# Performance work log

Hardware: AMD Instinct MI355X
Metric: run time of the kernel (lower is better)

## Reference

```python
import jax, jax.numpy as jnp
import numpy as np

T, B = 64, 256
VOCAB, D, H = 32000, 512, 1024


def setup_inputs() -> dict:
    key = jax.random.key(0)
    k1, k2, k3, k4 = jax.random.split(key, 4)
    x = jax.random.randint(k1, (T, B), 0, VOCAB)  # token 0 = padding
    embed = jax.random.normal(k2, (VOCAB, D), dtype=jnp.float32)
    w_i = jax.random.normal(k3, (D, 3 * H), dtype=jnp.float32) / np.sqrt(D)
    w_h = jax.random.normal(k4, (H, 3 * H), dtype=jnp.float32) / np.sqrt(H)
    b = jnp.zeros((3 * H,), dtype=jnp.float32)
    return {"x": x, "embed": embed, "w_i": w_i, "w_h": w_h, "b": b}


def reference(x, embed, w_i, w_h, b):
    # Embed and mask out padding token 0.  words: [T, B, D]
    words = embed[x] * (x > 0).astype(embed.dtype)[..., None]
    h_dim = w_h.shape[0]
    w_h_zr, w_h_a = w_h[:, : 2 * h_dim], w_h[:, 2 * h_dim :]
    b_zr, b_a = b[: 2 * h_dim], b[2 * h_dim :]

    def step(h, w_t):
        gx = w_t @ w_i  # [B, 3H]
        zr_x, a_x = gx[..., : 2 * h_dim], gx[..., 2 * h_dim :]
        zr = jax.nn.sigmoid(zr_x + h @ w_h_zr + b_zr)
        z, r = zr[..., :h_dim], zr[..., h_dim:]
        a = jnp.tanh(a_x + (r * h) @ w_h_a + b_a)
        h_new = (1.0 - z) * h + z * a
        return h_new, h_new

    h0 = jnp.zeros((x.shape[1], h_dim), dtype=embed.dtype)
    _, seq = jax.lax.scan(step, h0, words)  # seq: [T, B, H]
    return seq.sum(0)  # compress == 'sum' -> [B, H]
```

## Files before the change

### kernel.cpp

```cpp
#include <hip/hip_runtime.h>
#include <hip/hip_bf16.h>
#include <stdint.h>


#define TT 64
#define BB 256
#define DD 512
#define HH 1024
#define N3H 3072

using frag  = __attribute__((ext_vector_type(8))) short;
using f32x4 = __attribute__((ext_vector_type(4))) float;

__device__ __forceinline__ uint16_t f2b(float f) {
    uint32_t u = __builtin_bit_cast(uint32_t, f);
    uint32_t r = u + 0x7FFFu + ((u >> 16) & 1u);
    return (uint16_t)(r >> 16);
}
__device__ __forceinline__ float b2f(uint16_t b) {
    uint32_t u = ((uint32_t)b) << 16;
    return __builtin_bit_cast(float, u);
}

__device__ __forceinline__ void load8_l3(const uint16_t* p, frag* f) {
    asm volatile(
        "global_load_dwordx4 %0, %8, off sc0 sc1\n\t"
        "global_load_dwordx4 %1, %8, off offset:64 sc0 sc1\n\t"
        "global_load_dwordx4 %2, %8, off offset:128 sc0 sc1\n\t"
        "global_load_dwordx4 %3, %8, off offset:192 sc0 sc1\n\t"
        "global_load_dwordx4 %4, %8, off offset:256 sc0 sc1\n\t"
        "global_load_dwordx4 %5, %8, off offset:320 sc0 sc1\n\t"
        "global_load_dwordx4 %6, %8, off offset:384 sc0 sc1\n\t"
        "global_load_dwordx4 %7, %8, off offset:448 sc0 sc1\n\t"
        "s_waitcnt vmcnt(0)"
        : "=&v"(f[0]), "=&v"(f[1]), "=&v"(f[2]), "=&v"(f[3]),
          "=&v"(f[4]), "=&v"(f[5]), "=&v"(f[6]), "=&v"(f[7])
        : "v"(p)
        : "memory");
}


__global__ __launch_bounds__(256) void k_gather(const int* __restrict__ x,
                                                const float* __restrict__ embed,
                                                uint16_t* __restrict__ words) {
    int tid = blockIdx.x * 256 + threadIdx.x;
    int row = tid >> 6;
    int c8  = (tid & 63) << 3;
    int tok = x[row];
    float s = (tok > 0) ? 1.f : 0.f;
    const float4* src = (const float4*)(embed + (int64_t)tok * DD + c8);
    float4 v0 = src[0], v1 = src[1];
    float vals[8] = {v0.x, v0.y, v0.z, v0.w, v1.x, v1.y, v1.z, v1.w};
    union { uint16_t u[8]; uint4 q; } pk;
#pragma unroll
    for (int i = 0; i < 8; ++i) pk.u[i] = f2b(vals[i] * s);
    *(uint4*)(words + ((int64_t)row << 9) + c8) = pk.q;
}

__global__ void k_transpose(const float* __restrict__ src, uint16_t* __restrict__ dst,
                            int K, int N) {
    __shared__ float tile[32][33];
    int n0 = blockIdx.x * 32, k0 = blockIdx.y * 32;
    int tx = threadIdx.x, ty = threadIdx.y;
#pragma unroll
    for (int i = 0; i < 32; i += 8)
        tile[ty + i][tx] = src[(int64_t)(k0 + ty + i) * N + n0 + tx];
    __syncthreads();
#pragma unroll
    for (int i = 0; i < 32; i += 8)
        dst[(int64_t)(n0 + ty + i) * K + k0 + tx] = f2b(tile[tx][ty + i]);
}

__global__ void k_zero(uint4* p, int n16) {
    int i = blockIdx.x * blockDim.x + threadIdx.x;
    if (i < n16) p[i] = uint4{0u, 0u, 0u, 0u};
}


__global__ __launch_bounds__(256) void k_gemm_gx(const uint16_t* __restrict__ A,
                                                 const uint16_t* __restrict__ BT,
                                                 const float* __restrict__ bias,
                                                 uint16_t* __restrict__ C) {
    __shared__ uint16_t As[128][72];
    __shared__ uint16_t Bs[128][72];
    int m0 = blockIdx.y * 128;
    int n0 = blockIdx.x * 128;
    int t = threadIdx.x;
    int wave = t >> 6, lane = t & 63, quad = lane >> 4, l16 = lane & 15;
    int wm = (wave & 1) * 64, wn = (wave >> 1) * 64;
    f32x4 acc[4][4] = {};

    int sr = t >> 1;
    int sc = (t & 1) * 32;

    for (int k0 = 0; k0 < DD; k0 += 64) {
        const uint4* ga = (const uint4*)(A + (int64_t)(m0 + sr) * DD + k0 + sc);
        uint4 a0 = ga[0], a1 = ga[1], a2 = ga[2], a3 = ga[3];
        const uint4* gb = (const uint4*)(BT + (int64_t)(n0 + sr) * DD + k0 + sc);
        uint4 b0 = gb[0], b1 = gb[1], b2 = gb[2], b3 = gb[3];
        __syncthreads();
        *(uint4*)&As[sr][sc]      = a0;
        *(uint4*)&As[sr][sc + 8]  = a1;
        *(uint4*)&As[sr][sc + 16] = a2;
        *(uint4*)&As[sr][sc + 24] = a3;
        *(uint4*)&Bs[sr][sc]      = b0;
        *(uint4*)&Bs[sr][sc + 8]  = b1;
        *(uint4*)&Bs[sr][sc + 16] = b2;
        *(uint4*)&Bs[sr][sc + 24] = b3;
        __syncthreads();
#pragma unroll
        for (int kk = 0; kk < 64; kk += 32) {
            frag af[4], bf[4];
#pragma unroll
            for (int mi = 0; mi < 4; ++mi)
                af[mi] = *(const frag*)&As[wm + mi * 16 + l16][kk + quad * 8];
#pragma unroll
            for (int ni = 0; ni < 4; ++ni)
                bf[ni] = *(const frag*)&Bs[wn + ni * 16 + l16][kk + quad * 8];
#pragma unroll
            for (int mi = 0; mi < 4; ++mi)
#pragma unroll
                for (int ni = 0; ni < 4; ++ni)
                    acc[mi][ni] = __builtin_amdgcn_mfma_f32_16x16x32_bf16(
                        af[mi], bf[ni], acc[mi][ni], 0, 0, 0);
        }
    }
#pragma unroll
    for (int ni = 0; ni < 4; ++ni) {
        int col = n0 + wn + ni * 16 + l16;
        float bv = bias[col];
#pragma unroll
        for (int mi = 0; mi < 4; ++mi)
#pragma unroll
            for (int r = 0; r < 4; ++r) {
                int row = m0 + wm + mi * 16 + quad * 4 + r;
                C[(int64_t)row * N3H + col] = f2b(acc[mi][ni][r] + bv);
            }
    }
}


__global__ __launch_bounds__(256, 1) void k_recur(const uint16_t* __restrict__ gx,
                                                  const uint16_t* __restrict__ wht,
                                                  uint16_t* __restrict__ hbuf,
                                                  uint16_t* __restrict__ rhbuf,
                                                  unsigned int* __restrict__ bar,
                                                  float* __restrict__ out) {
    extern __shared__ uint16_t Wh[];
    const int LDW = HH + 8;
    int mg = blockIdx.x;
    int jb = blockIdx.y;
    int j0 = jb * 16;
    int m0 = mg * 64;
    int t = threadIdx.x, wave = t >> 6, lane = t & 63, quad = lane >> 4, l16 = lane & 15;

    for (int c = t; c < 48 * 128; c += 256) {
        int row = c >> 7;
        int off = (c & 127) << 3;
        int s = row >> 4, i = row & 15;
        *(uint4*)(Wh + row * LDW + off) =
            *(const uint4*)(wht + (int64_t)(s * HH + j0 + i) * HH + off);
    }
    __syncthreads();

    float hp[4]   = {0.f, 0.f, 0.f, 0.f};
    float zg[4];
    float osum[4] = {0.f, 0.f, 0.f, 0.f};
    int brow = m0 + wave * 16 + quad * 4;
    int jcol = j0 + l16;
    const int jc4 = j0 + (l16 & ~3);
    unsigned int* flags = bar + mg * 1024;
    unsigned int phase = 0;

    const uint16_t* harow  = hbuf  + (int64_t)(m0 + wave * 16 + l16) * HH + quad * 8;
    const uint16_t* rharow = rhbuf + (int64_t)(m0 + wave * 16 + l16) * HH + quad * 8;

    auto bar_arrive = [&]() {
        __syncthreads();
        if (t == 0)
            (void)__hip_atomic_fetch_add(&flags[jb * 16], 1u, __ATOMIC_RELAXED,
                                         __HIP_MEMORY_SCOPE_AGENT);
    };
    auto bar_wait = [&](unsigned int ph) {
        if (wave == 0) {
            long guard = 0;
            for (;;) {
                unsigned int v = __hip_atomic_load(&flags[lane * 16], __ATOMIC_RELAXED,
                                                   __HIP_MEMORY_SCOPE_AGENT);
                if (__all((int)(v >= ph))) break;
                __builtin_amdgcn_s_sleep(1);
                if (++guard > (1L << 13)) break;
            }
        }
        __syncthreads();
    };

    auto store4 = [&](uint16_t* base, int r, uint32_t mine) {
        uint32_t p2 = mine | (((uint32_t)__shfl_xor((int)mine, 1)) << 16);
        uint32_t hi = (uint32_t)__shfl_xor((int)p2, 2);
        if ((l16 & 3) == 0) {
            uint64_t p4 = (uint64_t)p2 | ((uint64_t)hi << 32);
            uint64_t* dst = (uint64_t*)base + (int64_t)(brow + r) * (HH / 4) + (jc4 >> 2);
            (void)__hip_atomic_exchange(dst, p4, __ATOMIC_RELAXED, __HIP_MEMORY_SCOPE_AGENT);
        }
    };

    for (int step = 0; step < TT; ++step) {
        if (step > 0) bar_arrive();

        uint16_t gzv[4], grv[4], gav[4];
        {
            const uint16_t* gxrow = gx + (int64_t)step * BB * N3H;
#pragma unroll
            for (int r = 0; r < 4; ++r) {
                const uint16_t* g = gxrow + (int64_t)(brow + r) * N3H + jcol;
                gzv[r] = g[0]; grv[r] = g[HH]; gav[r] = g[2 * HH];
            }
        }

        if (step > 0) bar_wait(++phase);

        {
            f32x4 acc0 = {}, acc1 = {};
            frag af[8];
#pragma unroll
            for (int kb = 0; kb < 4; ++kb) {
                load8_l3(harow + kb * 256, af);
#pragma unroll
                for (int j = 0; j < 8; ++j) {
                    int kk = kb * 8 + j;
                    frag b0 = *(const frag*)(Wh + (l16)      * LDW + kk * 32 + quad * 8);
                    frag b1 = *(const frag*)(Wh + (16 + l16) * LDW + kk * 32 + quad * 8);
                    acc0 = __builtin_amdgcn_mfma_f32_16x16x32_bf16(af[j], b0, acc0, 0, 0, 0);
                    acc1 = __builtin_amdgcn_mfma_f32_16x16x32_bf16(af[j], b1, acc1, 0, 0, 0);
                }
            }
#pragma unroll
            for (int r = 0; r < 4; ++r) {
                float zp = b2f(gzv[r]) + acc0[r];
                float rp = b2f(grv[r]) + acc1[r];
                float z  = 1.f / (1.f + __expf(-zp));
                float rg = 1.f / (1.f + __expf(-rp));
                zg[r] = z;
                store4(rhbuf, r, f2b(rg * hp[r]));
            }
        }

        bar_arrive();
        bar_wait(++phase);

        {
            f32x4 acc2 = {};
            frag af[8];
#pragma unroll
            for (int kb = 0; kb < 4; ++kb) {
                load8_l3(rharow + kb * 256, af);
#pragma unroll
                for (int j = 0; j < 8; ++j) {
                    int kk = kb * 8 + j;
                    frag b2 = *(const frag*)(Wh + (32 + l16) * LDW + kk * 32 + quad * 8);
                    acc2 = __builtin_amdgcn_mfma_f32_16x16x32_bf16(af[j], b2, acc2, 0, 0, 0);
                }
            }
#pragma unroll
            for (int r = 0; r < 4; ++r) {
                float a  = tanhf(b2f(gav[r]) + acc2[r]);
                float hn = (1.f - zg[r]) * hp[r] + zg[r] * a;
                osum[r] += hn;
                hp[r] = hn;
                store4(hbuf, r, f2b(hn));
            }
        }
    }
#pragma unroll
    for (int r = 0; r < 4; ++r)
        out[(int64_t)(brow + r) * HH + jcol] = osum[r];
}


extern "C" void kernel_launch(void* const* d_in, const int* in_sizes, int n_in,
                              void* d_out, int out_size, void* d_ws, size_t ws_size,
                              hipStream_t stream) {
    const int*   x     = (const int*)d_in[0];
    const float* embed = (const float*)d_in[1];
    const float* w_i   = (const float*)d_in[2];
    const float* w_h   = (const float*)d_in[3];
    const float* bias  = (const float*)d_in[4];
    float* out = (float*)d_out;

    char* ws = (char*)d_ws;
    uint16_t* gx    = (uint16_t*)(ws);
    uint16_t* wit   = (uint16_t*)(ws + 100663296);
    uint16_t* wht   = (uint16_t*)(ws + 103809024);
    uint16_t* words = (uint16_t*)(ws + 110100480);
    uint16_t* hbuf  = (uint16_t*)(ws + 126877696);
    uint16_t* rhbuf = (uint16_t*)(ws + 127401984);
    unsigned int* flags = (unsigned int*)(ws + 127926272);

    k_gather<<<4096, 256, 0, stream>>>(x, embed, words);
    k_transpose<<<dim3(96, 16), dim3(32, 8), 0, stream>>>(w_i, wit, DD, N3H);
    k_transpose<<<dim3(96, 32), dim3(32, 8), 0, stream>>>(w_h, wht, HH, N3H);
    k_zero<<<261, 256, 0, stream>>>((uint4*)(ws + 126877696), (1048576 + 16384) / 16);
    k_gemm_gx<<<dim3(24, 128), 256, 0, stream>>>(words, wit, bias, gx);
    k_recur<<<dim3(4, 64), 256, 48 * (HH + 8) * 2, stream>>>(gx, wht, hbuf, rhbuf, flags, out);
}
```

Baseline: 970.1 us.

## Split recurrent GRU kernel into z/r and candidate role blocks with pipelined loads

The persistent recurrent kernel is split into two block roles. One role computes the z/r gates and the other computes the candidate activation and hidden update, each covering 32 hidden columns. They exchange z values and previous h through new global shipping buffers and separate flag sets, so only one cross-block wait remains per phase instead of two full barriers per step. The h/rh loads for all K chunks are now issued up front and consumed with staggered waitcnts, overlapping memory latency with MFMA. This adds more global traffic for the handoff buffers and a more intricate synchronisation protocol that reuses the words buffer region.

```diff
diff --git a/kernel.cpp b/kernel.cpp
--- a/kernel.cpp
+++ b/kernel.cpp
@@ -11,6 +11,7 @@
 
 using frag  = __attribute__((ext_vector_type(8))) short;
 using f32x4 = __attribute__((ext_vector_type(4))) float;
+using u32x4 = __attribute__((ext_vector_type(4))) unsigned int;
 
 __device__ __forceinline__ uint16_t f2b(float f) {
     uint32_t u = __builtin_bit_cast(uint32_t, f);
@@ -22,7 +23,7 @@
     return __builtin_bit_cast(float, u);
 }
 
-__device__ __forceinline__ void load8_l3(const uint16_t* p, frag* f) {
+__device__ __forceinline__ void load8_issue(const uint16_t* p, frag* f) {
     asm volatile(
         "global_load_dwordx4 %0, %8, off sc0 sc1\n\t"
         "global_load_dwordx4 %1, %8, off offset:64 sc0 sc1\n\t"
@@ -31,13 +32,58 @@
         "global_load_dwordx4 %4, %8, off offset:256 sc0 sc1\n\t"
         "global_load_dwordx4 %5, %8, off offset:320 sc0 sc1\n\t"
         "global_load_dwordx4 %6, %8, off offset:384 sc0 sc1\n\t"
-        "global_load_dwordx4 %7, %8, off offset:448 sc0 sc1\n\t"
-        "s_waitcnt vmcnt(0)"
+        "global_load_dwordx4 %7, %8, off offset:448 sc0 sc1"
         : "=&v"(f[0]), "=&v"(f[1]), "=&v"(f[2]), "=&v"(f[3]),
           "=&v"(f[4]), "=&v"(f[5]), "=&v"(f[6]), "=&v"(f[7])
         : "v"(p)
         : "memory");
 }
+__device__ __forceinline__ void load16_l3(const void* p, u32x4* q) {
+    asm volatile("global_load_dwordx4 %0, %1, off sc0 sc1"
+                 : "=&v"(*q) : "v"(p) : "memory");
+}
+__device__ __forceinline__ void load32_l3(const void* p, f32x4* q0, f32x4* q1) {
+    asm volatile("global_load_dwordx4 %0, %2, off sc0 sc1\n\t"
+                 "global_load_dwordx4 %1, %2, off offset:16 sc0 sc1"
+                 : "=&v"(*q0), "=&v"(*q1) : "v"(p) : "memory");
+}
+__device__ __forceinline__ void exch64(uint64_t* dst, uint64_t v) {
+    (void)__hip_atomic_exchange(dst, v, __ATOMIC_RELAXED, __HIP_MEMORY_SCOPE_AGENT);
+}
+__device__ __forceinline__ uint64_t pkf(float a, float b) {
+    return (uint64_t)__builtin_bit_cast(uint32_t, a) |
+           ((uint64_t)__builtin_bit_cast(uint32_t, b) << 32);
+}
+
+#define WAIT8(N, F)                                                       \
+    asm volatile("s_waitcnt vmcnt(" #N ")"                                \
+                 : "+v"((F)[0]), "+v"((F)[1]), "+v"((F)[2]),              \
+                   "+v"((F)[3]), "+v"((F)[4]), "+v"((F)[5]),              \
+                   "+v"((F)[6]), "+v"((F)[7]))
+
+#define ZCONSUME(KB, HF)                                                          \
+    _Pragma("unroll")                                                             \
+    for (int j = 0; j < 8; ++j) {                                                 \
+        const uint16_t* wrow = Wh + ((KB) * 8 + j) * 32 + quad * 8;               \
+        frag bz0 = *(const frag*)(wrow + l16 * LDW);                              \
+        frag bz1 = *(const frag*)(wrow + (16 + l16) * LDW);                       \
+        frag br0 = *(const frag*)(wrow + (32 + l16) * LDW);                       \
+        frag br1 = *(const frag*)(wrow + (48 + l16) * LDW);                       \
+        accz0 = __builtin_amdgcn_mfma_f32_16x16x32_bf16((HF)[j], bz0, accz0, 0, 0, 0); \
+        accz1 = __builtin_amdgcn_mfma_f32_16x16x32_bf16((HF)[j], bz1, accz1, 0, 0, 0); \
+        accr0 = __builtin_amdgcn_mfma_f32_16x16x32_bf16((HF)[j], br0, accr0, 0, 0, 0); \
+        accr1 = __builtin_amdgcn_mfma_f32_16x16x32_bf16((HF)[j], br1, accr1, 0, 0, 0); \
+    }
+
+#define ACONSUME(KB, RF)                                                          \
+    _Pragma("unroll")                                                             \
+    for (int j = 0; j < 8; ++j) {                                                 \
+        const uint16_t* wrow = Wh + ((KB) * 8 + j) * 32 + quad * 8;               \
+        frag ba0 = *(const frag*)(wrow + l16 * LDW);                              \
+        frag ba1 = *(const frag*)(wrow + (16 + l16) * LDW);                       \
+        acca0 = __builtin_amdgcn_mfma_f32_16x16x32_bf16((RF)[j], ba0, acca0, 0, 0, 0); \
+        acca1 = __builtin_amdgcn_mfma_f32_16x16x32_bf16((RF)[j], ba1, acca1, 0, 0, 0); \
+    }
 
 
 __global__ __launch_bounds__(256) void k_gather(const int* __restrict__ x,
@@ -144,48 +190,44 @@
                                                   const uint16_t* __restrict__ wht,
                                                   uint16_t* __restrict__ hbuf,
                                                   uint16_t* __restrict__ rhbuf,
+                                                  float* __restrict__ zship,
+                                                  uint16_t* __restrict__ hship,
                                                   unsigned int* __restrict__ bar,
                                                   float* __restrict__ out) {
     extern __shared__ uint16_t Wh[];
     const int LDW = HH + 8;
-    int mg = blockIdx.x;
-    int jb = blockIdx.y;
-    int j0 = jb * 16;
+    int mg   = blockIdx.x >> 1;
+    int role = blockIdx.x & 1;
+    int jb   = blockIdx.y;
+    int j0 = jb * 32;
     int m0 = mg * 64;
     int t = threadIdx.x, wave = t >> 6, lane = t & 63, quad = lane >> 4, l16 = lane & 15;
-
-    for (int c = t; c < 48 * 128; c += 256) {
-        int row = c >> 7;
-        int off = (c & 127) << 3;
-        int s = row >> 4, i = row & 15;
-        *(uint4*)(Wh + row * LDW + off) =
-            *(const uint4*)(wht + (int64_t)(s * HH + j0 + i) * HH + off);
+    int brow = m0 + wave * 16 + quad * 4;
+
+    unsigned int* zfl = bar + mg * 512;
+    unsigned int* afl = bar + 2048 + mg * 512;
+    unsigned int* myf = (role == 0 ? zfl : afl) + jb * 16;
+
+    if (role == 0) {
+        for (int c = t; c < 64 * 128; c += 256) {
+            int row = c >> 7, off = (c & 127) << 3;
+            int o = (row < 32) ? (j0 + row) : (HH + j0 + row - 32);
+            *(uint4*)(Wh + row * LDW + off) = *(const uint4*)(wht + (int64_t)o * HH + off);
+        }
+    } else {
+        for (int c = t; c < 32 * 128; c += 256) {
+            int row = c >> 7, off = (c & 127) << 3;
+            int o = 2 * HH + j0 + row;
+            *(uint4*)(Wh + row * LDW + off) = *(const uint4*)(wht + (int64_t)o * HH + off);
+        }
     }
     __syncthreads();
 
-    float hp[4]   = {0.f, 0.f, 0.f, 0.f};
-    float zg[4];
-    float osum[4] = {0.f, 0.f, 0.f, 0.f};
-    int brow = m0 + wave * 16 + quad * 4;
-    int jcol = j0 + l16;
-    const int jc4 = j0 + (l16 & ~3);
-    unsigned int* flags = bar + mg * 1024;
-    unsigned int phase = 0;
-
-    const uint16_t* harow  = hbuf  + (int64_t)(m0 + wave * 16 + l16) * HH + quad * 8;
-    const uint16_t* rharow = rhbuf + (int64_t)(m0 + wave * 16 + l16) * HH + quad * 8;
-
-    auto bar_arrive = [&]() {
-        __syncthreads();
-        if (t == 0)
-            (void)__hip_atomic_fetch_add(&flags[jb * 16], 1u, __ATOMIC_RELAXED,
-                                         __HIP_MEMORY_SCOPE_AGENT);
-    };
-    auto bar_wait = [&](unsigned int ph) {
+    auto wait_all = [&](unsigned int* fl, unsigned int ph) {
         if (wave == 0) {
             long guard = 0;
             for (;;) {
-                unsigned int v = __hip_atomic_load(&flags[lane * 16], __ATOMIC_RELAXED,
+                unsigned int v = __hip_atomic_load(&fl[(lane & 31) * 16], __ATOMIC_RELAXED,
                                                    __HIP_MEMORY_SCOPE_AGENT);
                 if (__all((int)(v >= ph))) break;
                 __builtin_amdgcn_s_sleep(1);
@@ -194,87 +236,127 @@
         }
         __syncthreads();
     };
-
-    auto store4 = [&](uint16_t* base, int r, uint32_t mine) {
+    auto arrive = [&]() {
+        __syncthreads();
+        if (t == 0)
+            (void)__hip_atomic_fetch_add(myf, 1u, __ATOMIC_RELAXED, __HIP_MEMORY_SCOPE_AGENT);
+    };
+    auto store4 = [&](uint16_t* base, int row, int jc4, uint32_t mine) {
         uint32_t p2 = mine | (((uint32_t)__shfl_xor((int)mine, 1)) << 16);
         uint32_t hi = (uint32_t)__shfl_xor((int)p2, 2);
         if ((l16 & 3) == 0) {
             uint64_t p4 = (uint64_t)p2 | ((uint64_t)hi << 32);
-            uint64_t* dst = (uint64_t*)base + (int64_t)(brow + r) * (HH / 4) + (jc4 >> 2);
+            uint64_t* dst = (uint64_t*)base + (int64_t)row * (HH / 4) + (jc4 >> 2);
             (void)__hip_atomic_exchange(dst, p4, __ATOMIC_RELAXED, __HIP_MEMORY_SCOPE_AGENT);
         }
     };
 
-    for (int step = 0; step < TT; ++step) {
-        if (step > 0) bar_arrive();
-
-        uint16_t gzv[4], grv[4], gav[4];
-        {
+    size_t sidx = (size_t)((mg * 32 + jb) * 256 + t);
+
+    if (role == 0) {
+        const uint16_t* harow = hbuf + (int64_t)(m0 + wave * 16 + l16) * HH + quad * 8;
+        const uint16_t* hs = hship + (sidx << 3);
+        uint64_t* zb = (uint64_t*)zship + (sidx << 2);
+        for (int step = 0; step < TT; ++step) {
+            float gzv[2][4], grv[2][4];
             const uint16_t* gxrow = gx + (int64_t)step * BB * N3H;
 #pragma unroll
-            for (int r = 0; r < 4; ++r) {
-                const uint16_t* g = gxrow + (int64_t)(brow + r) * N3H + jcol;
-                gzv[r] = g[0]; grv[r] = g[HH]; gav[r] = g[2 * HH];
-            }
-        }
-
-        if (step > 0) bar_wait(++phase);
-
-        {
-            f32x4 acc0 = {}, acc1 = {};
-            frag af[8];
-#pragma unroll
-            for (int kb = 0; kb < 4; ++kb) {
-                load8_l3(harow + kb * 256, af);
-#pragma unroll
-                for (int j = 0; j < 8; ++j) {
-                    int kk = kb * 8 + j;
-                    frag b0 = *(const frag*)(Wh + (l16)      * LDW + kk * 32 + quad * 8);
-                    frag b1 = *(const frag*)(Wh + (16 + l16) * LDW + kk * 32 + quad * 8);
-                    acc0 = __builtin_amdgcn_mfma_f32_16x16x32_bf16(af[j], b0, acc0, 0, 0, 0);
-                    acc1 = __builtin_amdgcn_mfma_f32_16x16x32_bf16(af[j], b1, acc1, 0, 0, 0);
+            for (int ni = 0; ni < 2; ++ni)
+#pragma unroll
+                for (int r = 0; r < 4; ++r) {
+                    const uint16_t* g = gxrow + (int64_t)(brow + r) * N3H + j0 + ni * 16 + l16;
+                    gzv[ni][r] = b2f(g[0]);
+                    grv[ni][r] = b2f(g[HH]);
                 }
-            }
-#pragma unroll
-            for (int r = 0; r < 4; ++r) {
-                float zp = b2f(gzv[r]) + acc0[r];
-                float rp = b2f(grv[r]) + acc1[r];
-                float z  = 1.f / (1.f + __expf(-zp));
-                float rg = 1.f / (1.f + __expf(-rp));
-                zg[r] = z;
-                store4(rhbuf, r, f2b(rg * hp[r]));
-            }
-        }
-
-        bar_arrive();
-        bar_wait(++phase);
-
-        {
-            f32x4 acc2 = {};
-            frag af[8];
-#pragma unroll
-            for (int kb = 0; kb < 4; ++kb) {
-                load8_l3(rharow + kb * 256, af);
-#pragma unroll
-                for (int j = 0; j < 8; ++j) {
-                    int kk = kb * 8 + j;
-                    frag b2 = *(const frag*)(Wh + (32 + l16) * LDW + kk * 32 + quad * 8);
-                    acc2 = __builtin_amdgcn_mfma_f32_16x16x32_bf16(af[j], b2, acc2, 0, 0, 0);
+            if (step > 0) wait_all(afl, (unsigned)step);
+            asm volatile("s_waitcnt vmcnt(0)" ::: "memory");
+            frag h0[8], h1[8], h2[8], h3[8];
+            load8_issue(harow,       h0);
+            load8_issue(harow + 256, h1);
+            load8_issue(harow + 512, h2);
+            load8_issue(harow + 768, h3);
+            u32x4 hq;
+            load16_l3(hs, &hq);
+            f32x4 accz0 = {}, accz1 = {}, accr0 = {}, accr1 = {};
+            WAIT8(25, h0); ZCONSUME(0, h0);
+            WAIT8(17, h1); ZCONSUME(1, h1);
+            WAIT8(9,  h2); ZCONSUME(2, h2);
+            WAIT8(1,  h3); ZCONSUME(3, h3);
+            asm volatile("s_waitcnt vmcnt(0)" : "+v"(hq));
+            float zf[2][4];
+#pragma unroll
+            for (int ni = 0; ni < 2; ++ni)
+#pragma unroll
+                for (int r = 0; r < 4; ++r) {
+                    float zp = gzv[ni][r] + ((ni == 0) ? accz0 : accz1)[r];
+                    float rp = grv[ni][r] + ((ni == 0) ? accr0 : accr1)[r];
+                    float z  = 1.f / (1.f + __expf(-zp));
+                    float rg = 1.f / (1.f + __expf(-rp));
+                    zf[ni][r] = z;
+                    uint32_t w = hq[ni * 2 + (r >> 1)];
+                    uint16_t hb16 = (r & 1) ? (uint16_t)(w >> 16) : (uint16_t)(w & 0xFFFFu);
+                    store4(rhbuf, brow + r, j0 + ni * 16 + (l16 & ~3),
+                           (uint32_t)f2b(rg * b2f(hb16)));
                 }
-            }
-#pragma unroll
-            for (int r = 0; r < 4; ++r) {
-                float a  = tanhf(b2f(gav[r]) + acc2[r]);
-                float hn = (1.f - zg[r]) * hp[r] + zg[r] * a;
-                osum[r] += hn;
-                hp[r] = hn;
-                store4(hbuf, r, f2b(hn));
-            }
-        }
-    }
-#pragma unroll
-    for (int r = 0; r < 4; ++r)
-        out[(int64_t)(brow + r) * HH + jcol] = osum[r];
+            exch64(zb + 0, pkf(zf[0][0], zf[0][1]));
+            exch64(zb + 1, pkf(zf[0][2], zf[0][3]));
+            exch64(zb + 2, pkf(zf[1][0], zf[1][1]));
+            exch64(zb + 3, pkf(zf[1][2], zf[1][3]));
+            arrive();
+        }
+    } else {
+        const uint16_t* rharow = rhbuf + (int64_t)(m0 + wave * 16 + l16) * HH + quad * 8;
+        const float* zsrc = zship + (sidx << 3);
+        uint64_t* hsb = (uint64_t*)hship + (sidx << 1);
+        float hp[2][4] = {}, osum[2][4] = {};
+        for (int step = 0; step < TT; ++step) {
+            float gav[2][4];
+            const uint16_t* gxrow = gx + (int64_t)step * BB * N3H;
+#pragma unroll
+            for (int ni = 0; ni < 2; ++ni)
+#pragma unroll
+                for (int r = 0; r < 4; ++r)
+                    gav[ni][r] = b2f(gxrow[(int64_t)(brow + r) * N3H + 2 * HH + j0 + ni * 16 + l16]);
+            wait_all(zfl, (unsigned)(step + 1));
+            asm volatile("s_waitcnt vmcnt(0)" ::: "memory");
+            frag rf0[8], rf1[8], rf2[8], rf3[8];
+            load8_issue(rharow,       rf0);
+            load8_issue(rharow + 256, rf1);
+            load8_issue(rharow + 512, rf2);
+            load8_issue(rharow + 768, rf3);
+            f32x4 zq0, zq1;
+            load32_l3(zsrc, &zq0, &zq1);
+            f32x4 acca0 = {}, acca1 = {};
+            WAIT8(26, rf0); ACONSUME(0, rf0);
+            WAIT8(18, rf1); ACONSUME(1, rf1);
+            WAIT8(10, rf2); ACONSUME(2, rf2);
+            WAIT8(2,  rf3); ACONSUME(3, rf3);
+            asm volatile("s_waitcnt vmcnt(0)" : "+v"(zq0), "+v"(zq1));
+            uint16_t hb[2][4];
+#pragma unroll
+            for (int ni = 0; ni < 2; ++ni)
+#pragma unroll
+                for (int r = 0; r < 4; ++r) {
+                    float a = tanhf(gav[ni][r] + ((ni == 0) ? acca0 : acca1)[r]);
+                    float z = (ni == 0) ? zq0[r] : zq1[r];
+                    float hn = (1.f - z) * hp[ni][r] + z * a;
+                    osum[ni][r] += hn;
+                    hp[ni][r] = hn;
+                    hb[ni][r] = f2b(hn);
+                    store4(hbuf, brow + r, j0 + ni * 16 + (l16 & ~3), (uint32_t)hb[ni][r]);
+                }
+            exch64(hsb + 0, (uint64_t)(hb[0][0] | ((uint32_t)hb[0][1] << 16)) |
+                            ((uint64_t)(hb[0][2] | ((uint32_t)hb[0][3] << 16)) << 32));
+            exch64(hsb + 1, (uint64_t)(hb[1][0] | ((uint32_t)hb[1][1] << 16)) |
+                            ((uint64_t)(hb[1][2] | ((uint32_t)hb[1][3] << 16)) << 32));
+            arrive();
+        }
+#pragma unroll
+        for (int ni = 0; ni < 2; ++ni)
+#pragma unroll
+            for (int r = 0; r < 4; ++r)
+                out[(int64_t)(brow + r) * HH + j0 + ni * 16 + l16] = osum[ni][r];
+    }
 }
 
 
@@ -293,6 +375,8 @@
     uint16_t* wit   = (uint16_t*)(ws + 100663296);
     uint16_t* wht   = (uint16_t*)(ws + 103809024);
     uint16_t* words = (uint16_t*)(ws + 110100480);
+    float*    zship = (float*)(ws + 110100480);
+    uint16_t* hship = (uint16_t*)(ws + 111149056);
     uint16_t* hbuf  = (uint16_t*)(ws + 126877696);
     uint16_t* rhbuf = (uint16_t*)(ws + 127401984);
     unsigned int* flags = (unsigned int*)(ws + 127926272);
@@ -302,5 +386,7 @@
     k_transpose<<<dim3(96, 32), dim3(32, 8), 0, stream>>>(w_h, wht, HH, N3H);
     k_zero<<<261, 256, 0, stream>>>((uint4*)(ws + 126877696), (1048576 + 16384) / 16);
     k_gemm_gx<<<dim3(24, 128), 256, 0, stream>>>(words, wit, bias, gx);
-    k_recur<<<dim3(4, 64), 256, 48 * (HH + 8) * 2, stream>>>(gx, wht, hbuf, rhbuf, flags, out);
-}
+    k_zero<<<128, 256, 0, stream>>>((uint4*)(ws + 111149056), 524288 / 16);
+    k_recur<<<dim3(8, 32), 256, 64 * (HH + 8) * 2, stream>>>(gx, wht, hbuf, rhbuf,
+                                                             zship, hship, flags, out);
+}
```

Result: slower. 1.278 ms (+31.8%).

## Read recurrent state from XCD-local L2 mirror when producer blocks share the XCD

Applied to the files above, without the earlier changes.

Remaps the recurrent grid so that groups of 32 column blocks tend to land on the same XCD, records each block's XCC ID, and checks at startup whether all producers of each half of K sit on the reader's XCD. Each h and r*h value is also written with a plain store to a second mirror buffer. When the producers are local, the fragments are read with sc0-only loads (L2-cached) instead of sc0 sc1 system-coherent loads. All four K-chunk loads are now issued up front and waited on incrementally with vmcnt, so memory latency overlaps the MFMA work. The cost is doubled state stores, a startup barrier, and a dependence on the hardware's block-to-XCD placement, which is not guaranteed; if the producers are not local, the code falls back to the coherent path.

```diff
diff --git a/kernel.cpp b/kernel.cpp
--- a/kernel.cpp
+++ b/kernel.cpp
@@ -22,7 +22,7 @@
     return __builtin_bit_cast(float, u);
 }
 
-__device__ __forceinline__ void load8_l3(const uint16_t* p, frag* f) {
+__device__ __forceinline__ void load8_issue(const uint16_t* p, frag* f) {
     asm volatile(
         "global_load_dwordx4 %0, %8, off sc0 sc1\n\t"
         "global_load_dwordx4 %1, %8, off offset:64 sc0 sc1\n\t"
@@ -31,13 +31,51 @@
         "global_load_dwordx4 %4, %8, off offset:256 sc0 sc1\n\t"
         "global_load_dwordx4 %5, %8, off offset:320 sc0 sc1\n\t"
         "global_load_dwordx4 %6, %8, off offset:384 sc0 sc1\n\t"
-        "global_load_dwordx4 %7, %8, off offset:448 sc0 sc1\n\t"
-        "s_waitcnt vmcnt(0)"
+        "global_load_dwordx4 %7, %8, off offset:448 sc0 sc1"
         : "=&v"(f[0]), "=&v"(f[1]), "=&v"(f[2]), "=&v"(f[3]),
           "=&v"(f[4]), "=&v"(f[5]), "=&v"(f[6]), "=&v"(f[7])
         : "v"(p)
         : "memory");
 }
+__device__ __forceinline__ void load8_issue_loc(const uint16_t* p, frag* f) {
+    asm volatile(
+        "global_load_dwordx4 %0, %8, off sc0\n\t"
+        "global_load_dwordx4 %1, %8, off offset:64 sc0\n\t"
+        "global_load_dwordx4 %2, %8, off offset:128 sc0\n\t"
+        "global_load_dwordx4 %3, %8, off offset:192 sc0\n\t"
+        "global_load_dwordx4 %4, %8, off offset:256 sc0\n\t"
+        "global_load_dwordx4 %5, %8, off offset:320 sc0\n\t"
+        "global_load_dwordx4 %6, %8, off offset:384 sc0\n\t"
+        "global_load_dwordx4 %7, %8, off offset:448 sc0"
+        : "=&v"(f[0]), "=&v"(f[1]), "=&v"(f[2]), "=&v"(f[3]),
+          "=&v"(f[4]), "=&v"(f[5]), "=&v"(f[6]), "=&v"(f[7])
+        : "v"(p)
+        : "memory");
+}
+
+#define WAIT8(N, F)                                                       \
+    asm volatile("s_waitcnt vmcnt(" #N ")"                                \
+                 : "+v"((F)[0]), "+v"((F)[1]), "+v"((F)[2]),              \
+                   "+v"((F)[3]), "+v"((F)[4]), "+v"((F)[5]),              \
+                   "+v"((F)[6]), "+v"((F)[7]))
+
+#define ZCON(KB, HF)                                                              \
+    _Pragma("unroll")                                                             \
+    for (int j = 0; j < 8; ++j) {                                                 \
+        int kk = (KB) * 8 + j;                                                    \
+        frag b0 = *(const frag*)(Wh + (l16)      * LDW + kk * 32 + quad * 8);     \
+        frag b1 = *(const frag*)(Wh + (16 + l16) * LDW + kk * 32 + quad * 8);     \
+        acc0 = __builtin_amdgcn_mfma_f32_16x16x32_bf16((HF)[j], b0, acc0, 0, 0, 0); \
+        acc1 = __builtin_amdgcn_mfma_f32_16x16x32_bf16((HF)[j], b1, acc1, 0, 0, 0); \
+    }
+
+#define ACON(KB, RF)                                                              \
+    _Pragma("unroll")                                                             \
+    for (int j = 0; j < 8; ++j) {                                                 \
+        int kk = (KB) * 8 + j;                                                    \
+        frag b2 = *(const frag*)(Wh + (32 + l16) * LDW + kk * 32 + quad * 8);     \
+        acc2 = __builtin_amdgcn_mfma_f32_16x16x32_bf16((RF)[j], b2, acc2, 0, 0, 0); \
+    }
 
 
 __global__ __launch_bounds__(256) void k_gather(const int* __restrict__ x,
@@ -144,12 +182,17 @@
                                                   const uint16_t* __restrict__ wht,
                                                   uint16_t* __restrict__ hbuf,
                                                   uint16_t* __restrict__ rhbuf,
+                                                  uint16_t* __restrict__ hbufL2,
+                                                  uint16_t* __restrict__ rhbufL2,
+                                                  unsigned int* __restrict__ xtab,
                                                   unsigned int* __restrict__ bar,
+                                                  unsigned int* __restrict__ bar2,
                                                   float* __restrict__ out) {
     extern __shared__ uint16_t Wh[];
     const int LDW = HH + 8;
-    int mg = blockIdx.x;
-    int jb = blockIdx.y;
+    int mgx = blockIdx.x;
+    int mg  = mgx & 3;
+    int jb  = (mgx >> 2) * 32 + blockIdx.y;
     int j0 = jb * 16;
     int m0 = mg * 64;
     int t = threadIdx.x, wave = t >> 6, lane = t & 63, quad = lane >> 4, l16 = lane & 15;
@@ -161,7 +204,40 @@
         *(uint4*)(Wh + row * LDW + off) =
             *(const uint4*)(wht + (int64_t)(s * HH + j0 + i) * HH + off);
     }
+
+    unsigned int myxcd;
+    asm("s_getreg_b32 %0, hwreg(HW_REG_XCC_ID)" : "=s"(myxcd));
+    if (t == 0)
+        (void)__hip_atomic_exchange(&xtab[mg * 64 + jb], myxcd, __ATOMIC_RELAXED,
+                                    __HIP_MEMORY_SCOPE_AGENT);
     __syncthreads();
+    if (t == 0)
+        (void)__hip_atomic_fetch_add(&bar2[mg * 1024 + jb * 16], 1u, __ATOMIC_RELAXED,
+                                     __HIP_MEMORY_SCOPE_AGENT);
+    if (wave == 0) {
+        long guard = 0;
+        for (;;) {
+            unsigned int v = __hip_atomic_load(&bar2[mg * 1024 + lane * 16],
+                                               __ATOMIC_RELAXED, __HIP_MEMORY_SCOPE_AGENT);
+            if (__all((int)(v >= 1u))) break;
+            __builtin_amdgcn_s_sleep(1);
+            if (++guard > (1L << 13)) break;
+        }
+    }
+    __syncthreads();
+    bool loc01, loc23;
+    {
+        unsigned int tv;
+        asm volatile("global_load_dword %0, %1, off sc0 sc1\n\t"
+                     "s_waitcnt vmcnt(0)"
+                     : "=v"(tv) : "v"(xtab + mg * 64 + lane) : "memory");
+        unsigned int c0 = (unsigned int)__shfl((int)tv, 0);
+        unsigned int c1 = (unsigned int)__shfl((int)tv, 32);
+        bool eq = tv == ((lane < 32) ? c0 : c1);
+        uint64_t bal = __ballot(eq);
+        loc01 = ((bal & 0xFFFFFFFFull) == 0xFFFFFFFFull) && (c0 == myxcd);
+        loc23 = ((bal >> 32) == 0xFFFFFFFFull) && (c1 == myxcd);
+    }
 
     float hp[4]   = {0.f, 0.f, 0.f, 0.f};
     float zg[4];
@@ -172,8 +248,11 @@
     unsigned int* flags = bar + mg * 1024;
     unsigned int phase = 0;
 
-    const uint16_t* harow  = hbuf  + (int64_t)(m0 + wave * 16 + l16) * HH + quad * 8;
-    const uint16_t* rharow = rhbuf + (int64_t)(m0 + wave * 16 + l16) * HH + quad * 8;
+    const int64_t arow = (int64_t)(m0 + wave * 16 + l16) * HH + quad * 8;
+    const uint16_t* harow   = hbuf    + arow;
+    const uint16_t* harowL  = hbufL2  + arow;
+    const uint16_t* rharow  = rhbuf   + arow;
+    const uint16_t* rharowL = rhbufL2 + arow;
 
     auto bar_arrive = [&]() {
         __syncthreads();
@@ -195,13 +274,15 @@
         __syncthreads();
     };
 
-    auto store4 = [&](uint16_t* base, int r, uint32_t mine) {
+    auto store4 = [&](uint16_t* base, uint16_t* baseL2, int r, uint32_t mine) {
         uint32_t p2 = mine | (((uint32_t)__shfl_xor((int)mine, 1)) << 16);
         uint32_t hi = (uint32_t)__shfl_xor((int)p2, 2);
         if ((l16 & 3) == 0) {
             uint64_t p4 = (uint64_t)p2 | ((uint64_t)hi << 32);
-            uint64_t* dst = (uint64_t*)base + (int64_t)(brow + r) * (HH / 4) + (jc4 >> 2);
-            (void)__hip_atomic_exchange(dst, p4, __ATOMIC_RELAXED, __HIP_MEMORY_SCOPE_AGENT);
+            int64_t idx = (int64_t)(brow + r) * (HH / 4) + (jc4 >> 2);
+            (void)__hip_atomic_exchange((uint64_t*)base + idx, p4, __ATOMIC_RELAXED,
+                                        __HIP_MEMORY_SCOPE_AGENT);
+            *((uint64_t*)baseL2 + idx) = p4;
         }
     };
 
@@ -219,22 +300,19 @@
         }
 
         if (step > 0) bar_wait(++phase);
+        asm volatile("s_waitcnt vmcnt(0)" ::: "memory");
 
         {
+            frag h0[8], h1[8], h2[8], h3[8];
+            if (loc01) { load8_issue_loc(harowL,       h0); load8_issue_loc(harowL + 256, h1); }
+            else       { load8_issue(harow,            h0); load8_issue(harow + 256,      h1); }
+            if (loc23) { load8_issue_loc(harowL + 512, h2); load8_issue_loc(harowL + 768, h3); }
+            else       { load8_issue(harow + 512,      h2); load8_issue(harow + 768,      h3); }
             f32x4 acc0 = {}, acc1 = {};
-            frag af[8];
-#pragma unroll
-            for (int kb = 0; kb < 4; ++kb) {
-                load8_l3(harow + kb * 256, af);
-#pragma unroll
-                for (int j = 0; j < 8; ++j) {
-                    int kk = kb * 8 + j;
-                    frag b0 = *(const frag*)(Wh + (l16)      * LDW + kk * 32 + quad * 8);
-                    frag b1 = *(const frag*)(Wh + (16 + l16) * LDW + kk * 32 + quad * 8);
-                    acc0 = __builtin_amdgcn_mfma_f32_16x16x32_bf16(af[j], b0, acc0, 0, 0, 0);
-                    acc1 = __builtin_amdgcn_mfma_f32_16x16x32_bf16(af[j], b1, acc1, 0, 0, 0);
-                }
-            }
+            WAIT8(24, h0); ZCON(0, h0);
+            WAIT8(16, h1); ZCON(1, h1);
+            WAIT8(8,  h2); ZCON(2, h2);
+            WAIT8(0,  h3); ZCON(3, h3);
 #pragma unroll
             for (int r = 0; r < 4; ++r) {
                 float zp = b2f(gzv[r]) + acc0[r];
@@ -242,33 +320,32 @@
                 float z  = 1.f / (1.f + __expf(-zp));
                 float rg = 1.f / (1.f + __expf(-rp));
                 zg[r] = z;
-                store4(rhbuf, r, f2b(rg * hp[r]));
+                store4(rhbuf, rhbufL2, r, (uint32_t)f2b(rg * hp[r]));
             }
         }
 
         bar_arrive();
         bar_wait(++phase);
+        asm volatile("s_waitcnt vmcnt(0)" ::: "memory");
 
         {
+            frag rf0[8], rf1[8], rf2[8], rf3[8];
+            if (loc01) { load8_issue_loc(rharowL,       rf0); load8_issue_loc(rharowL + 256, rf1); }
+            else       { load8_issue(rharow,            rf0); load8_issue(rharow + 256,      rf1); }
+            if (loc23) { load8_issue_loc(rharowL + 512, rf2); load8_issue_loc(rharowL + 768, rf3); }
+            else       { load8_issue(rharow + 512,      rf2); load8_issue(rharow + 768,      rf3); }
             f32x4 acc2 = {};
-            frag af[8];
-#pragma unroll
-            for (int kb = 0; kb < 4; ++kb) {
-                load8_l3(rharow + kb * 256, af);
-#pragma unroll
-                for (int j = 0; j < 8; ++j) {
-                    int kk = kb * 8 + j;
-                    frag b2 = *(const frag*)(Wh + (32 + l16) * LDW + kk * 32 + quad * 8);
-                    acc2 = __builtin_amdgcn_mfma_f32_16x16x32_bf16(af[j], b2, acc2, 0, 0, 0);
-                }
-            }
+            WAIT8(24, rf0); ACON(0, rf0);
+            WAIT8(16, rf1); ACON(1, rf1);
+            WAIT8(8,  rf2); ACON(2, rf2);
+            WAIT8(0,  rf3); ACON(3, rf3);
 #pragma unroll
             for (int r = 0; r < 4; ++r) {
                 float a  = tanhf(b2f(gav[r]) + acc2[r]);
                 float hn = (1.f - zg[r]) * hp[r] + zg[r] * a;
                 osum[r] += hn;
                 hp[r] = hn;
-                store4(hbuf, r, f2b(hn));
+                store4(hbuf, hbufL2, r, (uint32_t)f2b(hn));
             }
         }
     }
@@ -293,6 +370,10 @@
     uint16_t* wit   = (uint16_t*)(ws + 100663296);
     uint16_t* wht   = (uint16_t*)(ws + 103809024);
     uint16_t* words = (uint16_t*)(ws + 110100480);
+    uint16_t* hbufL2  = (uint16_t*)(ws + 110100480);
+    uint16_t* rhbufL2 = (uint16_t*)(ws + 110624768);
+    unsigned int* bar2 = (unsigned int*)(ws + 111149056);
+    unsigned int* xtab = (unsigned int*)(ws + 111165440);
     uint16_t* hbuf  = (uint16_t*)(ws + 126877696);
     uint16_t* rhbuf = (uint16_t*)(ws + 127401984);
     unsigned int* flags = (unsigned int*)(ws + 127926272);
@@ -302,5 +383,8 @@
     k_transpose<<<dim3(96, 32), dim3(32, 8), 0, stream>>>(w_h, wht, HH, N3H);
     k_zero<<<261, 256, 0, stream>>>((uint4*)(ws + 126877696), (1048576 + 16384) / 16);
     k_gemm_gx<<<dim3(24, 128), 256, 0, stream>>>(words, wit, bias, gx);
-    k_recur<<<dim3(4, 64), 256, 48 * (HH + 8) * 2, stream>>>(gx, wht, hbuf, rhbuf, flags, out);
-}
+    k_zero<<<261, 256, 0, stream>>>((uint4*)(ws + 110100480), (524288 + 524288 + 16384 + 4096) / 16);
+    k_recur<<<dim3(8, 32), 256, 48 * (HH + 8) * 2, stream>>>(gx, wht, hbuf, rhbuf,
+                                                             hbufL2, rhbufL2, xtab,
+                                                             flags, bar2, out);
+}
```

After: 1.005 ms. 1.04x slower.
